# Kernel optimization log

Hardware: AMD Instinct MI355X
Metric: run time of the kernel (lower is better)

## Reference

```python
import jax, jax.numpy as jnp
import numpy as np

N, P, C, K = 16, 2048, 64, 16
EPS = 1e-5


def _bn(x, gamma, beta, axes):
    # training-mode batchnorm: biased variance over all dims except channel (last)
    m = jnp.mean(x, axis=axes, keepdims=True)
    v = jnp.var(x, axis=axes, keepdims=True)
    return (x - m) * jax.lax.rsqrt(v + EPS) * gamma + beta


def setup_inputs() -> dict:
    key = jax.random.key(0)
    ks = jax.random.split(key, 16)
    w = lambda k, shape: jax.random.normal(k, shape, jnp.float32) * 0.05
    inp = {"features": jax.random.normal(ks[0], (N, C, P), jnp.float32)}
    # edge-conv MLP: layer 0 takes 2*C input channels
    inp["w0"], inp["b0"] = w(ks[1], (C, 2 * C)), jnp.zeros((C,), jnp.float32)
    inp["g0"], inp["be0"] = jnp.ones((C,), jnp.float32), jnp.zeros((C,), jnp.float32)
    inp["w1"], inp["b1"] = w(ks[2], (C, C)), jnp.zeros((C,), jnp.float32)
    inp["g1"], inp["be1"] = jnp.ones((C,), jnp.float32), jnp.zeros((C,), jnp.float32)
    inp["w2"], inp["b2"] = w(ks[3], (C, C)), jnp.zeros((C,), jnp.float32)
    inp["g2"], inp["be2"] = jnp.ones((C,), jnp.float32), jnp.zeros((C,), jnp.float32)
    # shortcut 1x1 conv + BN
    inp["ws"], inp["bs"] = w(ks[4], (C, C)), jnp.zeros((C,), jnp.float32)
    inp["gs"], inp["bes"] = jnp.ones((C,), jnp.float32), jnp.zeros((C,), jnp.float32)
    return inp


def reference(features, w0, b0, g0, be0, w1, b1, g1, be1, w2, b2, g2, be2, ws, bs, gs, bes):
    # index != 0: features come in as (N, C, P) -> (N, P, C)
    X = jnp.transpose(features, (0, 2, 1))  # (N, P, C)

    # --- KNN via full pairwise squared distances ---
    r = jnp.sum(X * X, axis=-1)  # (N, P)
    d = r[:, :, None] - 2.0 * jnp.einsum('npc,nqc->npq', X, X) + r[:, None, :]
    _, idx = jax.lax.top_k(-d, K + 1)
    idx = idx[:, :, 1:]  # drop self, (N, P, K)

    # --- irregular gather + edge-feature concat ---
    f = X[jnp.arange(X.shape[0])[:, None, None], idx]  # (N, P, K, C)
    fc = jnp.broadcast_to(X[:, :, None, :], f.shape)   # center feature tiled
    h = jnp.concatenate([fc, fc - f], axis=-1)         # (N, P, K, 2C)

    def conv_bn_relu(h, w, b, g, be):
        h = jnp.einsum('npki,oi->npko', h, w) + b
        return jax.nn.relu(_bn(h, g, be, (0, 1, 2)))

    h = conv_bn_relu(h, w0, b0, g0, be0)
    h = conv_bn_relu(h, w1, b1, g1, be1)
    h = conv_bn_relu(h, w2, b2, g2, be2)
    h = jnp.mean(h, axis=2)  # aggregate over K -> (N, P, C)

    # shortcut: 1x1 conv + BN on center features
    sc = jnp.einsum('npi,oi->npo', X, ws) + bs
    sc = _bn(sc, gs, bes, (0, 1))

    out = jax.nn.relu(h + sc)           # (N, P, C)
    return jnp.transpose(out, (0, 2, 1))  # (N, C, P) to match torch layout
```

## Files before the change

### kernel.cpp

```cpp
#include <hip/hip_runtime.h>

using u16    = unsigned short;
using u32    = unsigned int;
using u64    = unsigned long long;
using bf16x8 = __attribute__((ext_vector_type(8))) short;
using f32x4  = __attribute__((ext_vector_type(4))) float;
using u16x4  = __attribute__((ext_vector_type(4))) u16;

#define NB   16
#define PP   2048
#define CC   64
#define KK   16
#define MROWS (NB*PP*KK)
#define NPTS  (NB*PP)

__device__ __forceinline__ float b2f(u16 u) { return __uint_as_float(((unsigned)u) << 16); }
__device__ __forceinline__ u16 f2b(float f) {
  unsigned u = __float_as_uint(f);
  return (u16)((u + 0x7fffu + ((u >> 16) & 1u)) >> 16);
}

__device__ __forceinline__ u64 dkey(float d, int qi) {
  unsigned u = __float_as_uint(d);
  u = u ^ (((unsigned)((int)u >> 31)) | 0x80000000u);
  return ((u64)u << 32) | (unsigned)qi;
}

template<bool UP>
__device__ __forceinline__ void ce(u64 &a, u64 &b) {
  const bool lt = a < b;
  const u64 lo = lt ? a : b;
  const u64 hi = lt ? b : a;
  if (UP) { a = lo; b = hi; } else { a = hi; b = lo; }
}

__device__ __forceinline__ void sort16(u64 (&v)[16]) {
  #pragma unroll
  for (int k = 2; k <= 16; k <<= 1) {
    #pragma unroll
    for (int j = k >> 1; j > 0; j >>= 1) {
      #pragma unroll
      for (int i = 0; i < 16; ++i) {
        const int l = i ^ j;
        if (l > i) {
          if ((i & k) == 0) ce<true>(v[i], v[l]);
          else              ce<false>(v[i], v[l]);
        }
      }
    }
  }
}

__device__ __forceinline__ void merge16(u64 (&dl)[16], const u64 (&nb)[16]) {
  u64 t[16];
  #pragma unroll
  for (int s = 0; s < 16; ++s) {
    const u64 a = dl[s], b = nb[15 - s];
    t[s] = a < b ? a : b;
  }
  #pragma unroll
  for (int j = 8; j > 0; j >>= 1) {
    #pragma unroll
    for (int i = 0; i < 16; ++i) {
      const int l = i ^ j;
      if (l > i) ce<true>(t[i], t[l]);
    }
  }
  #pragma unroll
  for (int s = 0; s < 16; ++s) dl[s] = t[s];
}

__global__ __launch_bounds__(256) void prep_k(const float* __restrict__ F,
                                              u16* __restrict__ Xb,
                                              u16* __restrict__ X3,
                                              float* __restrict__ r) {
  int gidx = blockIdx.x * 256 + threadIdx.x;
  int n = gidx >> 11, p = gidx & 2047;
  const float* src = F + (size_t)n * CC * PP + p;
  float rr = 0.f;
  u16 ha[CC], ma[CC], la[CC];
  #pragma unroll
  for (int c = 0; c < CC; ++c) {
    const float x = src[(size_t)c * PP];
    rr += x * x;
    const u16 h = f2b(x);
    const float eh = x - b2f(h);
    const u16 m = f2b(eh);
    const float el = eh - b2f(m);
    const u16 lo_ = f2b(el);
    ha[c] = h; ma[c] = m; la[c] = lo_;
  }
  u16* db = Xb + (size_t)gidx * CC;
  u16* d3 = X3 + (size_t)gidx * 128;
  #pragma unroll
  for (int c = 0; c < CC; c += 8) {
    bf16x8 wh, wm, wl;
    #pragma unroll
    for (int j = 0; j < 8; ++j) { wh[j] = (short)ha[c+j]; wm[j] = (short)ma[c+j]; wl[j] = (short)la[c+j]; }
    *(bf16x8*)(db + c)      = wh;
    *(bf16x8*)(d3 + c)      = wm;
    *(bf16x8*)(d3 + 64 + c) = wl;
  }
  r[gidx] = rr;
}

__global__ __launch_bounds__(256) void cvtw_k(const float* __restrict__ w0, const float* __restrict__ w1,
                                              const float* __restrict__ w2, const float* __restrict__ wsb,
                                              u16* __restrict__ b0, u16* __restrict__ b1,
                                              u16* __restrict__ b2, u16* __restrict__ bs) {
  int i = blockIdx.x * 256 + threadIdx.x;
  if (i < 8192)        b0[i]          = f2b(w0[i]);
  else if (i < 12288)  b1[i - 8192]   = f2b(w1[i - 8192]);
  else if (i < 16384)  b2[i - 12288]  = f2b(w2[i - 12288]);
  else if (i < 20480)  bs[i - 16384]  = f2b(wsb[i - 16384]);
}

__global__ __launch_bounds__(256)
void knn_k(const u16* __restrict__ Xb, const u16* __restrict__ X3,
           const float* __restrict__ r, u64* __restrict__ part) {
  __shared__ u16 XqL[128 * 200];
  float* D  = (float*)XqL;
  u64*   mb = (u64*)XqL;

  const int n  = blockIdx.x >> 7;
  const int pb = ((blockIdx.x >> 2) & 31) * 64;
  const int qq = blockIdx.x & 3;
  const int qstart = qq * 512;
  const int t  = threadIdx.x;
  const int l  = t & 63, w = t >> 6;
  const int lo = l & 15, hi4 = l >> 4;
  const int prow = t & 63;
  const int qh2  = t >> 6;
  const int u4   = (prow & 7) * 4;

  const u16*  Xbn = Xb + (size_t)(n * PP) * CC;
  const u16*  X3n = X3 + (size_t)(n * PP) * 128;
  const float* rb = r + n * PP;

  bf16x8 ah[2], am[2], al[2];
  {
    const size_t rowb = (size_t)(pb + w * 16 + lo);
    #pragma unroll
    for (int kb = 0; kb < 2; ++kb) {
      ah[kb] = *(const bf16x8*)(Xbn + rowb * CC  + kb * 32 + hi4 * 8);
      am[kb] = *(const bf16x8*)(X3n + rowb * 128 + kb * 32 + hi4 * 8);
      al[kb] = *(const bf16x8*)(X3n + rowb * 128 + 64 + kb * 32 + hi4 * 8);
    }
  }

  u64 dl[16];
  #pragma unroll
  for (int s = 0; s < 16; ++s) dl[s] = ~0ULL;

  #pragma unroll 1
  for (int qb = qstart; qb < qstart + 512; qb += 128) {
    __syncthreads();
    {
      #pragma unroll
      for (int k = 0; k < 4; ++k) {
        const int u = t + k * 256;
        const int row = u >> 3, unit = u & 7;
        *(bf16x8*)(XqL + row * 200 + unit * 8) =
          *(const bf16x8*)(Xbn + (size_t)(qb + row) * CC + unit * 8);
      }
      #pragma unroll
      for (int k = 0; k < 8; ++k) {
        const int u = t + k * 256;
        const int row = u >> 4, unit = u & 15;
        *(bf16x8*)(XqL + row * 200 + 64 + unit * 8) =
          *(const bf16x8*)(X3n + (size_t)(qb + row) * 128 + unit * 8);
      }
    }
    __syncthreads();

    f32x4 acc[8];
    #pragma unroll
    for (int Q = 0; Q < 8; ++Q) { f32x4 z = {0.f, 0.f, 0.f, 0.f}; acc[Q] = z; }

    #pragma unroll
    for (int Q = 0; Q < 8; ++Q) {
      const int qrow = Q * 16 + lo;
      #pragma unroll
      for (int kb = 0; kb < 2; ++kb) {
        const int base = qrow * 200 + kb * 32 + hi4 * 8;
        const bf16x8 bh = *(const bf16x8*)(XqL + base);
        const bf16x8 bm = *(const bf16x8*)(XqL + base + 64);
        const bf16x8 bl = *(const bf16x8*)(XqL + base + 128);
        acc[Q] = __builtin_amdgcn_mfma_f32_16x16x32_bf16(ah[kb], bh, acc[Q], 0, 0, 0);
        acc[Q] = __builtin_amdgcn_mfma_f32_16x16x32_bf16(am[kb], bh, acc[Q], 0, 0, 0);
        acc[Q] = __builtin_amdgcn_mfma_f32_16x16x32_bf16(ah[kb], bm, acc[Q], 0, 0, 0);
        acc[Q] = __builtin_amdgcn_mfma_f32_16x16x32_bf16(al[kb], bh, acc[Q], 0, 0, 0);
        acc[Q] = __builtin_amdgcn_mfma_f32_16x16x32_bf16(ah[kb], bl, acc[Q], 0, 0, 0);
        acc[Q] = __builtin_amdgcn_mfma_f32_16x16x32_bf16(am[kb], bm, acc[Q], 0, 0, 0);
      }
    }
    __syncthreads();

    {
      #pragma unroll
      for (int Q = 0; Q < 8; ++Q) {
        const int qloc  = Q * 16 + lo;
        const int qglob = qb + qloc;
        const float rq  = rb[qglob];
        const int bidx = qloc >> 2, qrem = qloc & 3;
        #pragma unroll
        for (int e = 0; e < 4; ++e) {
          const int p = w * 16 + hi4 * 4 + e;
          float d = rq - 2.f * acc[Q][e];
          if (qglob == pb + p) d = 3.0e38f;
          const int swz = ((bidx ^ ((p & 7) << 2)) << 2) + qrem;
          D[p * 132 + swz] = d;
        }
      }
    }
    __syncthreads();

    #pragma unroll
    for (int half = 0; half < 2; ++half) {
      u64 nb[16];
      const float* drow = D + (size_t)prow * 132;
      #pragma unroll
      for (int bb = 0; bb < 4; ++bb) {
        const int b = qh2 * 8 + half * 4 + bb;
        const float4 dv = *(const float4*)(drow + ((b ^ u4) * 4));
        const int qg = qb + b * 4;
        nb[bb*4+0] = dkey(dv.x, qg+0);
        nb[bb*4+1] = dkey(dv.y, qg+1);
        nb[bb*4+2] = dkey(dv.z, qg+2);
        nb[bb*4+3] = dkey(dv.w, qg+3);
      }
      sort16(nb);
      merge16(dl, nb);
    }
  }

  __syncthreads();
  {
    #pragma unroll
    for (int s = 0; s < 16; ++s) mb[s * 256 + t] = dl[s];
  }
  __syncthreads();
  if (t < 64) {
    #pragma unroll 1
    for (int j = 1; j < 4; ++j) {
      u64 nb[16];
      #pragma unroll
      for (int s = 0; s < 16; ++s) nb[s] = mb[s * 256 + (t + 64 * j)];
      merge16(dl, nb);
    }
    u64* outp = part + (((size_t)n * PP + pb + t) * 4 + qq) * 16;
    #pragma unroll
    for (int s = 0; s < 16; ++s) outp[s] = dl[s];
  }
}

__global__ __launch_bounds__(256) void knnm_k(const u64* __restrict__ part,
                                              int* __restrict__ idx) {
  const int row = blockIdx.x * 256 + threadIdx.x;
  const u64* p = part + (size_t)row * 64;
  u64 dl[16];
  #pragma unroll
  for (int s = 0; s < 16; ++s) dl[s] = p[s];
  #pragma unroll 1
  for (int j = 1; j < 4; ++j) {
    u64 nb[16];
    #pragma unroll
    for (int s = 0; s < 16; ++s) nb[s] = p[j * 16 + s];
    merge16(dl, nb);
  }
  #pragma unroll
  for (int s = 0; s < 16; ++s)
    idx[(size_t)row * KK + s] = (int)(dl[s] & 0xFFFFFFFFu);
}

template<int KIN, bool GATHER, bool BNRELU>
__global__ __launch_bounds__(256) void conv_k(const u16* __restrict__ in,
                                              const int* __restrict__ idxp,
                                              const u16* __restrict__ wb,
                                              const float* __restrict__ bias,
                                              const float* __restrict__ st,
                                              u16* __restrict__ yout,
                                              float* __restrict__ partials) {
  constexpr int NKB = KIN / 32;
  __shared__ float sred[4][4][32];
  const int t = threadIdx.x;
  const int wv = t >> 6, l = t & 63, hi = l >> 4, lo = l & 15;
  const int rbase = blockIdx.x * 256 + wv * 64;

  bf16x8 wf[4][NKB];
  #pragma unroll
  for (int ob = 0; ob < 4; ++ob)
    #pragma unroll
    for (int kb = 0; kb < NKB; ++kb)
      wf[ob][kb] = *(const bf16x8*)(wb + (size_t)(ob*16 + lo) * KIN + kb*32 + hi*8);

  int qv[4];
  if constexpr (GATHER) {
    #pragma unroll
    for (int rb = 0; rb < 4; ++rb) {
      const int g = (rbase + rb*16) >> 4;
      qv[rb] = idxp[g * KK + lo];
    }
  }

  f32x4 acc[4][4];
  #pragma unroll
  for (int a = 0; a < 4; ++a)
    #pragma unroll
    for (int b = 0; b < 4; ++b) { f32x4 z = {0.f, 0.f, 0.f, 0.f}; acc[a][b] = z; }

  #pragma unroll
  for (int kb = 0; kb < NKB; ++kb) {
    float sv[8], tv[8];
    if constexpr (BNRELU) {
      const int k0 = kb*32 + hi*8;
      *(float4*)&sv[0] = *(const float4*)(st + k0);
      *(float4*)&sv[4] = *(const float4*)(st + k0 + 4);
      *(float4*)&tv[0] = *(const float4*)(st + KIN + k0);
      *(float4*)&tv[4] = *(const float4*)(st + KIN + k0 + 4);
    }
    bf16x8 af[4];
    #pragma unroll
    for (int rb = 0; rb < 4; ++rb) {
      if constexpr (GATHER) {
        const int g  = (rbase + rb*16) >> 4;
        const int k0 = kb*32 + hi*8;
        const bf16x8 fc = *(const bf16x8*)(in + (size_t)g * CC + (k0 & 63));
        if (kb < 2) {
          af[rb] = fc;
        } else {
          const int nn = g >> 11;
          const bf16x8 fv = *(const bf16x8*)(in + (size_t)(nn * PP + qv[rb]) * CC + (k0 & 63));
          bf16x8 df;
          #pragma unroll
          for (int j = 0; j < 8; ++j)
            df[j] = (short)f2b(b2f((u16)fc[j]) - b2f((u16)fv[j]));
          af[rb] = df;
        }
      } else {
        const int row = rbase + rb*16 + lo;
        const bf16x8 rv = *(const bf16x8*)(in + (size_t)row * KIN + kb*32 + hi*8);
        if constexpr (BNRELU) {
          bf16x8 tr;
          #pragma unroll
          for (int j = 0; j < 8; ++j) {
            const float x = fmaxf(b2f((u16)rv[j]) * sv[j] + tv[j], 0.f);
            tr[j] = (short)f2b(x);
          }
          af[rb] = tr;
        } else {
          af[rb] = rv;
        }
      }
    }
    #pragma unroll
    for (int ob = 0; ob < 4; ++ob)
      #pragma unroll
      for (int rb = 0; rb < 4; ++rb)
        acc[rb][ob] = __builtin_amdgcn_mfma_f32_16x16x32_bf16(wf[ob][kb], af[rb], acc[rb][ob], 0, 0, 0);
  }

  float ssum[16], qsum[16];
  #pragma unroll
  for (int j = 0; j < 16; ++j) { ssum[j] = 0.f; qsum[j] = 0.f; }
  #pragma unroll
  for (int ob = 0; ob < 4; ++ob) {
    const int o0 = ob*16 + hi*4;
    const float4 bv = *(const float4*)(bias + o0);
    #pragma unroll
    for (int rb = 0; rb < 4; ++rb) {
      const int row = rbase + rb*16 + lo;
      const float v0 = acc[rb][ob][0] + bv.x;
      const float v1 = acc[rb][ob][1] + bv.y;
      const float v2 = acc[rb][ob][2] + bv.z;
      const float v3 = acc[rb][ob][3] + bv.w;
      u16x4 pk; pk[0] = f2b(v0); pk[1] = f2b(v1); pk[2] = f2b(v2); pk[3] = f2b(v3);
      *(u16x4*)(yout + (size_t)row * CC + o0) = pk;
      ssum[ob*4+0] += v0; qsum[ob*4+0] += v0*v0;
      ssum[ob*4+1] += v1; qsum[ob*4+1] += v1*v1;
      ssum[ob*4+2] += v2; qsum[ob*4+2] += v2*v2;
      ssum[ob*4+3] += v3; qsum[ob*4+3] += v3*v3;
    }
  }
  #pragma unroll
  for (int m = 1; m < 16; m <<= 1) {
    #pragma unroll
    for (int j = 0; j < 16; ++j) {
      ssum[j] += __shfl_xor(ssum[j], m, 64);
      qsum[j] += __shfl_xor(qsum[j], m, 64);
    }
  }
  if (lo == 0) {
    #pragma unroll
    for (int j = 0; j < 16; ++j) {
      sred[wv][hi][j*2]   = ssum[j];
      sred[wv][hi][j*2+1] = qsum[j];
    }
  }
  __syncthreads();
  if (t < 128) {
    const int c = t & 63, half = t >> 6;
    const int slot = ((c >> 4) * 4 + (c & 3)) * 2 + half;
    const int h2 = (c >> 2) & 3;
    const float v = sred[0][h2][slot] + sred[1][h2][slot] + sred[2][h2][slot] + sred[3][h2][slot];
    partials[(size_t)blockIdx.x * 128 + half * 64 + c] = v;
  }
}

__global__ __launch_bounds__(256) void red1_k(const float* __restrict__ partials,
                                              float* __restrict__ out, int nwg) {
  __shared__ float accs[2][128];
  const int t = threadIdx.x, e = t & 127, h = t >> 7;
  float s = 0.f;
  for (int w = blockIdx.x + h * 64; w < nwg; w += 128)
    s += partials[(size_t)w * 128 + e];
  accs[h][e] = s;
  __syncthreads();
  if (t < 128) out[(size_t)blockIdx.x * 128 + t] = accs[0][t] + accs[1][t];
}

__global__ __launch_bounds__(128) void red2_k(const float* __restrict__ p2,
                                              const float* __restrict__ g,
                                              const float* __restrict__ be,
                                              float* __restrict__ st, float invM) {
  __shared__ float sq[128];
  const int t = threadIdx.x;
  float s = 0.f;
  #pragma unroll 8
  for (int w = 0; w < 64; ++w) s += p2[w * 128 + t];
  sq[t] = s;
  __syncthreads();
  if (t < 64) {
    const float S = sq[t], Q = sq[64 + t];
    const float m = S * invM;
    const float v = fmaxf(Q * invM - m * m, 0.f);
    const float sc = g[t] * rsqrtf(v + 1e-5f);
    st[t] = sc;
    st[64 + t] = be[t] - m * sc;
  }
}

__global__ __launch_bounds__(256) void final_k(const u16* __restrict__ y2,
                                               const u16* __restrict__ ysc,
                                               const float* __restrict__ st2,
                                               const float* __restrict__ stS,
                                               float* __restrict__ out) {
  __shared__ float ot[64][68];
  const int b = blockIdx.x, t = threadIdx.x;
  const int n = b >> 5, p0 = (b & 31) * 64;
  const int phh = t >> 2, jh = t & 3, c0 = jh * 16;
  const int g = n * PP + p0 + phh;
  float acc[16];
  #pragma unroll
  for (int i = 0; i < 16; ++i) acc[i] = 0.f;
  float sv[16], tv[16];
  #pragma unroll
  for (int i = 0; i < 16; ++i) { sv[i] = st2[c0 + i]; tv[i] = st2[64 + c0 + i]; }
  for (int k = 0; k < KK; ++k) {
    const u16* rp = y2 + ((size_t)g * KK + k) * CC + c0;
    const bf16x8 v0 = *(const bf16x8*)rp;
    const bf16x8 v1 = *(const bf16x8*)(rp + 8);
    #pragma unroll
    for (int j = 0; j < 8; ++j) {
      acc[j]     += fmaxf(b2f((u16)v0[j]) * sv[j]     + tv[j],     0.f);
      acc[8 + j] += fmaxf(b2f((u16)v1[j]) * sv[8 + j] + tv[8 + j], 0.f);
    }
  }
  const u16* sp = ysc + (size_t)g * CC + c0;
  const bf16x8 s0 = *(const bf16x8*)sp;
  const bf16x8 s1 = *(const bf16x8*)(sp + 8);
  #pragma unroll
  for (int i = 0; i < 16; ++i) {
    const float scx = b2f((u16)(i < 8 ? s0[i] : s1[i - 8])) * stS[c0 + i] + stS[64 + c0 + i];
    ot[c0 + i][phh] = fmaxf(acc[i] * (1.f / 16.f) + scx, 0.f);
  }
  __syncthreads();
  const int c = t >> 2, pc = t & 3;
  const float* src = &ot[c][pc * 16];
  float* dst = out + (size_t)n * CC * PP + (size_t)c * PP + p0 + pc * 16;
  #pragma unroll
  for (int j = 0; j < 16; j += 4) *(float4*)(dst + j) = *(const float4*)(src + j);
}

extern "C" void kernel_launch(void* const* d_in, const int* in_sizes, int n_in,
                              void* d_out, int out_size, void* d_ws, size_t ws_size,
                              hipStream_t stream) {
  (void)in_sizes; (void)n_in; (void)out_size; (void)ws_size;
  const float* F   = (const float*)d_in[0];
  const float* w0  = (const float*)d_in[1];
  const float* b0  = (const float*)d_in[2];
  const float* g0  = (const float*)d_in[3];
  const float* be0 = (const float*)d_in[4];
  const float* w1  = (const float*)d_in[5];
  const float* b1  = (const float*)d_in[6];
  const float* g1  = (const float*)d_in[7];
  const float* be1 = (const float*)d_in[8];
  const float* w2  = (const float*)d_in[9];
  const float* b2  = (const float*)d_in[10];
  const float* g2  = (const float*)d_in[11];
  const float* be2 = (const float*)d_in[12];
  const float* wS  = (const float*)d_in[13];
  const float* bS  = (const float*)d_in[14];
  const float* gS  = (const float*)d_in[15];
  const float* beS = (const float*)d_in[16];

  char* ws = (char*)d_ws;
  size_t off = 0;
  auto carve = [&](size_t bytes) -> void* {
    void* p = ws + off;
    off += (bytes + 255) & ~(size_t)255;
    return p;
  };
  u16*   Xb       = (u16*)  carve((size_t)NPTS * CC * 2);
  u16*   X3       = (u16*)  carve((size_t)NPTS * 128 * 2);
  float* rr       = (float*)carve((size_t)NPTS * 4);
  int*   idx      = (int*)  carve((size_t)NPTS * KK * 4);
  u16*   wb0      = (u16*)  carve(8192 * 2);
  u16*   wb1      = (u16*)  carve(4096 * 2);
  u16*   wb2      = (u16*)  carve(4096 * 2);
  u16*   wbs      = (u16*)  carve(4096 * 2);
  u16*   y        = (u16*)  carve((size_t)MROWS * CC * 2);
  u16*   ysc      = (u16*)  carve((size_t)NPTS * CC * 2);
  float* partials = (float*)carve((size_t)2048 * 128 * 4);
  float* p2       = (float*)carve((size_t)64 * 128 * 4);
  float* st0      = (float*)carve(128 * 4);
  float* st1      = (float*)carve(128 * 4);
  float* st2      = (float*)carve(128 * 4);
  float* stS      = (float*)carve(128 * 4);

  u64* part = (u64*)y;

  prep_k<<<NPTS / 256, 256, 0, stream>>>(F, Xb, X3, rr);
  cvtw_k<<<80, 256, 0, stream>>>(w0, w1, w2, wS, wb0, wb1, wb2, wbs);
  knn_k<<<NB * 32 * 4, 256, 0, stream>>>(Xb, X3, rr, part);
  knnm_k<<<NPTS / 256, 256, 0, stream>>>(part, idx);

  conv_k<128, true,  false><<<MROWS / 256, 256, 0, stream>>>(Xb, idx, wb0, b0, nullptr, y, partials);
  red1_k<<<64, 256, 0, stream>>>(partials, p2, MROWS / 256);
  red2_k<<<1, 128, 0, stream>>>(p2, g0, be0, st0, 1.f / (float)MROWS);

  conv_k<64, false, true><<<MROWS / 256, 256, 0, stream>>>(y, nullptr, wb1, b1, st0, y, partials);
  red1_k<<<64, 256, 0, stream>>>(partials, p2, MROWS / 256);
  red2_k<<<1, 128, 0, stream>>>(p2, g1, be1, st1, 1.f / (float)MROWS);

  conv_k<64, false, true><<<MROWS / 256, 256, 0, stream>>>(y, nullptr, wb2, b2, st1, y, partials);
  red1_k<<<64, 256, 0, stream>>>(partials, p2, MROWS / 256);
  red2_k<<<1, 128, 0, stream>>>(p2, g2, be2, st2, 1.f / (float)MROWS);

  conv_k<64, false, false><<<NPTS / 256, 256, 0, stream>>>(Xb, nullptr, wbs, bS, nullptr, ysc, partials);
  red1_k<<<64, 256, 0, stream>>>(partials, p2, NPTS / 256);
  red2_k<<<1, 128, 0, stream>>>(p2, gS, beS, stS, 1.f / (float)NPTS);

  final_k<<<NB * (PP / 64), 256, 0, stream>>>(y, ysc, st2, stS, (float*)d_out);
}
```

Baseline: 390.0 us.

## Swap MFMA operands so distances land in registers, removing LDS transpose

The KNN kernel now swaps the A/B operands of the bf16 MFMA so each lane's accumulator holds distances for its own query point across four candidates. Keys are built directly from registers and fed to sort/merge, with no write to a swizzled LDS distance buffer, two barriers, and LDS reads. The final cross-thread merge is remapped so the lanes with hi4==0 gather the partial lists of the four lane groups for each point. Each point's partial list now covers an interleaved subset of candidates instead of a contiguous one, and the merge pattern changes to match.

```diff
diff --git a/kernel.cpp b/kernel.cpp
--- a/kernel.cpp
+++ b/kernel.cpp
@@ -119,8 +119,7 @@
 void knn_k(const u16* __restrict__ Xb, const u16* __restrict__ X3,
            const float* __restrict__ r, u64* __restrict__ part) {
   __shared__ u16 XqL[128 * 200];
-  float* D  = (float*)XqL;
-  u64*   mb = (u64*)XqL;
+  u64* mb = (u64*)XqL;
 
   const int n  = blockIdx.x >> 7;
   const int pb = ((blockIdx.x >> 2) & 31) * 64;
@@ -129,9 +128,7 @@
   const int t  = threadIdx.x;
   const int l  = t & 63, w = t >> 6;
   const int lo = l & 15, hi4 = l >> 4;
-  const int prow = t & 63;
-  const int qh2  = t >> 6;
-  const int u4   = (prow & 7) * 4;
+  const int prow = pb + w * 16 + lo;
 
   const u16*  Xbn = Xb + (size_t)(n * PP) * CC;
   const u16*  X3n = X3 + (size_t)(n * PP) * 128;
@@ -139,7 +136,7 @@
 
   bf16x8 ah[2], am[2], al[2];
   {
-    const size_t rowb = (size_t)(pb + w * 16 + lo);
+    const size_t rowb = (size_t)prow;
     #pragma unroll
     for (int kb = 0; kb < 2; ++kb) {
       ah[kb] = *(const bf16x8*)(Xbn + rowb * CC  + kb * 32 + hi4 * 8);
@@ -173,61 +170,36 @@
     }
     __syncthreads();
 
-    f32x4 acc[8];
-    #pragma unroll
-    for (int Q = 0; Q < 8; ++Q) { f32x4 z = {0.f, 0.f, 0.f, 0.f}; acc[Q] = z; }
-
-    #pragma unroll
-    for (int Q = 0; Q < 8; ++Q) {
-      const int qrow = Q * 16 + lo;
+    #pragma unroll
+    for (int half = 0; half < 2; ++half) {
+      u64 nb[16];
       #pragma unroll
-      for (int kb = 0; kb < 2; ++kb) {
-        const int base = qrow * 200 + kb * 32 + hi4 * 8;
-        const bf16x8 bh = *(const bf16x8*)(XqL + base);
-        const bf16x8 bm = *(const bf16x8*)(XqL + base + 64);
-        const bf16x8 bl = *(const bf16x8*)(XqL + base + 128);
-        acc[Q] = __builtin_amdgcn_mfma_f32_16x16x32_bf16(ah[kb], bh, acc[Q], 0, 0, 0);
-        acc[Q] = __builtin_amdgcn_mfma_f32_16x16x32_bf16(am[kb], bh, acc[Q], 0, 0, 0);
-        acc[Q] = __builtin_amdgcn_mfma_f32_16x16x32_bf16(ah[kb], bm, acc[Q], 0, 0, 0);
-        acc[Q] = __builtin_amdgcn_mfma_f32_16x16x32_bf16(al[kb], bh, acc[Q], 0, 0, 0);
-        acc[Q] = __builtin_amdgcn_mfma_f32_16x16x32_bf16(ah[kb], bl, acc[Q], 0, 0, 0);
-        acc[Q] = __builtin_amdgcn_mfma_f32_16x16x32_bf16(am[kb], bm, acc[Q], 0, 0, 0);
-      }
-    }
-    __syncthreads();
-
-    {
-      #pragma unroll
-      for (int Q = 0; Q < 8; ++Q) {
-        const int qloc  = Q * 16 + lo;
-        const int qglob = qb + qloc;
-        const float rq  = rb[qglob];
-        const int bidx = qloc >> 2, qrem = qloc & 3;
+      for (int Qi = 0; Qi < 4; ++Qi) {
+        const int Q = half * 4 + Qi;
+        f32x4 acc = {0.f, 0.f, 0.f, 0.f};
+        const int qrow = Q * 16 + lo;
+        #pragma unroll
+        for (int kb = 0; kb < 2; ++kb) {
+          const int base = qrow * 200 + kb * 32 + hi4 * 8;
+          const bf16x8 bh = *(const bf16x8*)(XqL + base);
+          const bf16x8 bm = *(const bf16x8*)(XqL + base + 64);
+          const bf16x8 bl = *(const bf16x8*)(XqL + base + 128);
+          acc = __builtin_amdgcn_mfma_f32_16x16x32_bf16(bh, ah[kb], acc, 0, 0, 0);
+          acc = __builtin_amdgcn_mfma_f32_16x16x32_bf16(bh, am[kb], acc, 0, 0, 0);
+          acc = __builtin_amdgcn_mfma_f32_16x16x32_bf16(bm, ah[kb], acc, 0, 0, 0);
+          acc = __builtin_amdgcn_mfma_f32_16x16x32_bf16(bh, al[kb], acc, 0, 0, 0);
+          acc = __builtin_amdgcn_mfma_f32_16x16x32_bf16(bl, ah[kb], acc, 0, 0, 0);
+          acc = __builtin_amdgcn_mfma_f32_16x16x32_bf16(bm, am[kb], acc, 0, 0, 0);
+        }
+        const int q0 = qb + Q * 16 + hi4 * 4;
+        const float4 rv = *(const float4*)(rb + q0);
         #pragma unroll
         for (int e = 0; e < 4; ++e) {
-          const int p = w * 16 + hi4 * 4 + e;
-          float d = rq - 2.f * acc[Q][e];
-          if (qglob == pb + p) d = 3.0e38f;
-          const int swz = ((bidx ^ ((p & 7) << 2)) << 2) + qrem;
-          D[p * 132 + swz] = d;
+          float d = ((const float*)&rv)[e] - 2.f * acc[e];
+          const int qg = q0 + e;
+          if (qg == prow) d = 3.0e38f;
+          nb[Qi * 4 + e] = dkey(d, qg);
         }
-      }
-    }
-    __syncthreads();
-
-    #pragma unroll
-    for (int half = 0; half < 2; ++half) {
-      u64 nb[16];
-      const float* drow = D + (size_t)prow * 132;
-      #pragma unroll
-      for (int bb = 0; bb < 4; ++bb) {
-        const int b = qh2 * 8 + half * 4 + bb;
-        const float4 dv = *(const float4*)(drow + ((b ^ u4) * 4));
-        const int qg = qb + b * 4;
-        nb[bb*4+0] = dkey(dv.x, qg+0);
-        nb[bb*4+1] = dkey(dv.y, qg+1);
-        nb[bb*4+2] = dkey(dv.z, qg+2);
-        nb[bb*4+3] = dkey(dv.w, qg+3);
       }
       sort16(nb);
       merge16(dl, nb);
@@ -240,15 +212,15 @@
     for (int s = 0; s < 16; ++s) mb[s * 256 + t] = dl[s];
   }
   __syncthreads();
-  if (t < 64) {
+  if (hi4 == 0) {
     #pragma unroll 1
     for (int j = 1; j < 4; ++j) {
       u64 nb[16];
       #pragma unroll
-      for (int s = 0; s < 16; ++s) nb[s] = mb[s * 256 + (t + 64 * j)];
+      for (int s = 0; s < 16; ++s) nb[s] = mb[s * 256 + (w * 64 + j * 16 + lo)];
       merge16(dl, nb);
     }
-    u64* outp = part + (((size_t)n * PP + pb + t) * 4 + qq) * 16;
+    u64* outp = part + (((size_t)n * PP + prow) * 4 + qq) * 16;
     #pragma unroll
     for (int s = 0; s < 16; ++s) outp[s] = dl[s];
   }
```

Result: slower. 487.1 us (+24.9%).
